# Optimization experiments

Measured on AMD Instinct MI355X. Metric: run time of the kernel, lower is better.

## Reference

```python
import jax, jax.numpy as jnp
import numpy as np

N_NODES = 89250
N_EDGES = 899756
IN_F = 500
HID = 256
N_CLS = 7


def setup_inputs() -> dict:
    key = jax.random.key(0)
    ks = jax.random.split(key, 12)
    x = jax.random.normal(ks[0], (N_NODES, IN_F), dtype=jnp.float32)
    edge_index = jax.random.randint(ks[1], (2, N_EDGES), 0, N_NODES, dtype=jnp.int32)
    edge_weight = jax.random.uniform(ks[2], (N_EDGES,), dtype=jnp.float32)
    def glorot(k, shape):
        fan_in, fan_out = shape
        s = (6.0 / (fan_in + fan_out)) ** 0.5
        return jax.random.uniform(k, shape, jnp.float32, -s, s)
    W1 = glorot(ks[3], (2 * IN_F, HID))
    b1 = jnp.zeros((HID,), jnp.float32)
    W2 = glorot(ks[4], (2 * HID, HID))
    b2 = jnp.zeros((HID,), jnp.float32)
    W3 = glorot(ks[5], (2 * HID, HID))
    b3 = jnp.zeros((HID,), jnp.float32)
    Wl = glorot(ks[6], (3 * HID, N_CLS))
    bl = jnp.zeros((N_CLS,), jnp.float32)
    return {"x": x, "edge_index": edge_index, "edge_weight": edge_weight,
            "W1": W1, "b1": b1, "W2": W2, "b2": b2, "W3": W3, "b3": b3,
            "Wl": Wl, "bl": bl}


def _sage_conv(x, src, dst, edge_weight, W, b, num_nodes):
    # legacy PyG SAGEConv(concat=True): mean-aggregate weighted neighbor msgs,
    # concat with root features, then single linear (2*in -> out). No self-loops.
    msg = x[src] * edge_weight[:, None]                                  # [E, F]
    agg = jax.ops.segment_sum(msg, dst, num_segments=num_nodes)          # [N, F]
    cnt = jax.ops.segment_sum(jnp.ones_like(edge_weight), dst, num_segments=num_nodes)
    agg = agg / jnp.maximum(cnt, 1.0)[:, None]                           # scatter_mean
    h = jnp.concatenate([x, agg], axis=-1)                               # [N, 2F]
    return h @ W + b


def reference(x, edge_index, edge_weight, W1, b1, W2, b2, W3, b3, Wl, bl):
    n = x.shape[0]
    src, dst = edge_index[0], edge_index[1]  # message flows source -> target
    x1 = jax.nn.relu(_sage_conv(x, src, dst, edge_weight, W1, b1, n))
    x2 = jax.nn.relu(_sage_conv(x1, src, dst, edge_weight, W2, b2, n))
    x3 = jax.nn.relu(_sage_conv(x2, src, dst, edge_weight, W3, b3, n))
    h = jnp.concatenate([x1, x2, x3], axis=-1)                            # [N, 3H]
    logits = h @ Wl + bl                                                  # [N, C]
    return jax.nn.log_softmax(logits, axis=-1)
```

## Files before the change

### kernel.cpp

```cpp
#include <hip/hip_runtime.h>
#include <hip/hip_bf16.h>

#define NN 89250
#define NE 899756
#define INF_ 500
#define HID 256
#define NCLS 7

typedef __attribute__((ext_vector_type(8))) short bf16x8;
typedef __attribute__((ext_vector_type(4))) float f32x4;

#define GL2LDS16(gp, lp)                                                        \
    __builtin_amdgcn_global_load_lds(                                           \
        (const __attribute__((address_space(1))) void*)(gp),                    \
        (__attribute__((address_space(3))) void*)(lp), 16, 0, 0)

static __device__ __forceinline__ float b2f(short s) {
    union { unsigned int u; float f; } v;
    v.u = ((unsigned int)(unsigned short)s) << 16;
    return v.f;
}

__global__ void hist_kernel(const int* __restrict__ dst, int* __restrict__ cnt, int E) {
    int e = blockIdx.x * 256 + threadIdx.x;
    if (e < E) atomicAdd(&cnt[dst[e]], 1);
}

__global__ __launch_bounds__(256) void scan1_kernel(const int* __restrict__ cnt,
                                                    int* __restrict__ loc,
                                                    int* __restrict__ bsum, int N) {
    __shared__ int sd[256];
    int b = blockIdx.x, tid = threadIdx.x;
    int base = b * 1024 + tid * 4;
    int v[4];
    int sum = 0;
#pragma unroll
    for (int k = 0; k < 4; k++) {
        int i = base + k;
        v[k] = (i < N) ? cnt[i] : 0;
        sum += v[k];
    }
    sd[tid] = sum;
    __syncthreads();
    for (int off = 1; off < 256; off <<= 1) {
        int add = (tid >= off) ? sd[tid - off] : 0;
        __syncthreads();
        sd[tid] += add;
        __syncthreads();
    }
    int run = sd[tid] - sum;
    if (tid == 255) bsum[b] = sd[255];
#pragma unroll
    for (int k = 0; k < 4; k++) {
        int i = base + k;
        if (i < N) loc[i] = run;
        run += v[k];
    }
}

__global__ __launch_bounds__(256) void scan2_kernel(int* __restrict__ bsum,
                                                    int* __restrict__ total, int nb) {
    __shared__ int sd[256];
    int tid = threadIdx.x;
    int v = (tid < nb) ? bsum[tid] : 0;
    sd[tid] = v;
    __syncthreads();
    for (int off = 1; off < 256; off <<= 1) {
        int add = (tid >= off) ? sd[tid - off] : 0;
        __syncthreads();
        sd[tid] += add;
        __syncthreads();
    }
    if (tid < nb) bsum[tid] = sd[tid] - v;
    if (tid == 255) *total = sd[255];
}

__global__ void scan3_kernel(const int* __restrict__ cnt, const int* __restrict__ loc,
                             const int* __restrict__ bsum, const int* __restrict__ total,
                             int* __restrict__ offs, int* __restrict__ cursor,
                             float* __restrict__ invc, int N) {
    int i = blockIdx.x * 256 + threadIdx.x;
    if (i < N) {
        int o = loc[i] + bsum[i >> 10];
        offs[i] = o;
        cursor[i] = o;
        invc[i] = 1.0f / fmaxf((float)cnt[i], 1.0f);
    }
    if (i == 0) offs[N] = *total;
}

__global__ void scatter_kernel(const int* __restrict__ src, const int* __restrict__ dst,
                               const float* __restrict__ w, int* __restrict__ cursor,
                               int* __restrict__ csr_src, float* __restrict__ csr_w, int E) {
    int e = blockIdx.x * 256 + threadIdx.x;
    if (e < E) {
        int d = dst[e];
        int pos = atomicAdd(&cursor[d], 1);
        csr_src[pos] = src[e];
        csr_w[pos] = w[e];
    }
}

__global__ void conv_x_kernel(const float* __restrict__ x, __hip_bfloat16* __restrict__ xb) {
    long long idx = (long long)blockIdx.x * 256 + threadIdx.x;
    if (idx >= (long long)NN * 128) return;
    int row = (int)(idx >> 7), slot = (int)(idx & 127);
    float4 v = make_float4(0.f, 0.f, 0.f, 0.f);
    if (slot < 125) v = *(const float4*)&x[(size_t)row * 500 + slot * 4];
    __hip_bfloat16* o = xb + (size_t)row * 512 + slot * 4;
    o[0] = __float2bfloat16(v.x);
    o[1] = __float2bfloat16(v.y);
    o[2] = __float2bfloat16(v.z);
    o[3] = __float2bfloat16(v.w);
}

__global__ void conv_w_kernel(const float* __restrict__ W, __hip_bfloat16* __restrict__ BT,
                              int K, int Kp) {
    int idx = blockIdx.x * 256 + threadIdx.x;
    if (idx >= 512 * Kp) return;
    int j = idx / Kp, k = idx - j * Kp;
    float v = (k < K) ? W[(size_t)(k + ((j >= 256) ? K : 0)) * 256 + (j & 255)] : 0.f;
    BT[idx] = __float2bfloat16(v);
}

__global__ __launch_bounds__(256, 2) void gemm_mfma(
    const __hip_bfloat16* __restrict__ A, const __hip_bfloat16* __restrict__ BT,
    const float* __restrict__ bias, float* __restrict__ S,
    __hip_bfloat16* __restrict__ T, int N, int K) {
    __shared__ short lA[128 * 64];
    __shared__ short lB[128 * 64];
    int tid = threadIdx.x;
    int row0 = blockIdx.x * 128;
    int col0 = blockIdx.y * 128;
    int w = tid >> 6, l = tid & 63;
    int wm = (w >> 1) * 64, wn = (w & 1) * 64;
    int lr = l & 15, lk = (l >> 4) * 8;

    const char* gA[4];
    const char* gB[4];
    int ls[4];
#pragma unroll
    for (int p = 0; p < 4; p++) {
        int s = tid + p * 256;
        int r = s >> 3, c = s & 7;
        int ga_row = row0 + r;
        if (ga_row > N - 1) ga_row = N - 1;
        gA[p] = (const char*)A + (size_t)ga_row * K * 2 + c * 16;
        gB[p] = (const char*)BT + (size_t)(col0 + r) * K * 2 + c * 16;
        ls[p] = s * 16;
    }

    f32x4 acc[4][4];
#pragma unroll
    for (int m = 0; m < 4; m++)
#pragma unroll
        for (int n = 0; n < 4; n++) acc[m][n] = (f32x4){0.f, 0.f, 0.f, 0.f};

    int KT = K >> 6;
    for (int kt = 0; kt < KT; kt++) {
        size_t koff = (size_t)kt * 128;
#pragma unroll
        for (int p = 0; p < 4; p++) GL2LDS16(gA[p] + koff, (char*)lA + ls[p]);
#pragma unroll
        for (int p = 0; p < 4; p++) GL2LDS16(gB[p] + koff, (char*)lB + ls[p]);
        __syncthreads();
#pragma unroll
        for (int kk = 0; kk < 64; kk += 32) {
            bf16x8 af[4], bfr[4];
#pragma unroll
            for (int m = 0; m < 4; m++)
                af[m] = *(const bf16x8*)&lA[(wm + m * 16 + lr) * 64 + kk + lk];
#pragma unroll
            for (int n = 0; n < 4; n++)
                bfr[n] = *(const bf16x8*)&lB[(wn + n * 16 + lr) * 64 + kk + lk];
#pragma unroll
            for (int m = 0; m < 4; m++)
#pragma unroll
                for (int n = 0; n < 4; n++)
                    acc[m][n] = __builtin_amdgcn_mfma_f32_16x16x32_bf16(af[m], bfr[n],
                                                                        acc[m][n], 0, 0, 0);
        }
        __syncthreads();
    }

    int crow_base = row0 + wm + (l >> 4) * 4;
    bool isT = (col0 >= 256);
#pragma unroll
    for (int n = 0; n < 4; n++) {
        int col = col0 + wn + n * 16 + lr;
        float bv = isT ? 0.f : bias[col];
#pragma unroll
        for (int m = 0; m < 4; m++) {
#pragma unroll
            for (int r = 0; r < 4; r++) {
                int row = crow_base + m * 16 + r;
                if (row < N) {
                    float v = acc[m][n][r] + bv;
                    if (isT)
                        T[(size_t)row * 256 + (col - 256)] = __float2bfloat16(v);
                    else
                        S[(size_t)row * 256 + col] = v;
                }
            }
        }
    }
}

__global__ __launch_bounds__(256) void agg_fused_kernel(
    const float* __restrict__ S, const __hip_bfloat16* __restrict__ T,
    const int* __restrict__ offs, const int* __restrict__ csr_src,
    const float* __restrict__ csr_w, const float* __restrict__ invc,
    const float* __restrict__ Wlc, __hip_bfloat16* __restrict__ act,
    float* __restrict__ logits, int N) {
    __shared__ float sW[HID * NCLS];
    for (int i = threadIdx.x; i < HID * NCLS; i += 256) sW[i] = Wlc[i];
    __syncthreads();

    int g = threadIdx.x >> 5, t = threadIdx.x & 31;
    int n = blockIdx.x * 8 + g;
    if (n >= N) return;
    int beg = offs[n], end = offs[n + 1];

    float acc[8] = {};
    int j = beg;
    for (; j + 4 <= end; j += 4) {
        int s0 = csr_src[j], s1 = csr_src[j + 1], s2 = csr_src[j + 2], s3 = csr_src[j + 3];
        float w0 = csr_w[j], w1 = csr_w[j + 1], w2 = csr_w[j + 2], w3 = csr_w[j + 3];
        bf16x8 r0 = *(const bf16x8*)&T[(size_t)s0 * 256 + t * 8];
        bf16x8 r1 = *(const bf16x8*)&T[(size_t)s1 * 256 + t * 8];
        bf16x8 r2 = *(const bf16x8*)&T[(size_t)s2 * 256 + t * 8];
        bf16x8 r3 = *(const bf16x8*)&T[(size_t)s3 * 256 + t * 8];
#pragma unroll
        for (int k = 0; k < 8; k++) {
            acc[k] += b2f(r0[k]) * w0;
            acc[k] += b2f(r1[k]) * w1;
            acc[k] += b2f(r2[k]) * w2;
            acc[k] += b2f(r3[k]) * w3;
        }
    }
    for (; j < end; j++) {
        int s0 = csr_src[j];
        float w0 = csr_w[j];
        bf16x8 r0 = *(const bf16x8*)&T[(size_t)s0 * 256 + t * 8];
#pragma unroll
        for (int k = 0; k < 8; k++) acc[k] += b2f(r0[k]) * w0;
    }

    float ic = invc[n];
    const float* Srow = S + (size_t)n * 256 + t * 8;
    float4 sv0 = *(const float4*)&Srow[0];
    float4 sv1 = *(const float4*)&Srow[4];
    float a[8];
    a[0] = fmaxf(sv0.x + acc[0] * ic, 0.f);
    a[1] = fmaxf(sv0.y + acc[1] * ic, 0.f);
    a[2] = fmaxf(sv0.z + acc[2] * ic, 0.f);
    a[3] = fmaxf(sv0.w + acc[3] * ic, 0.f);
    a[4] = fmaxf(sv1.x + acc[4] * ic, 0.f);
    a[5] = fmaxf(sv1.y + acc[5] * ic, 0.f);
    a[6] = fmaxf(sv1.z + acc[6] * ic, 0.f);
    a[7] = fmaxf(sv1.w + acc[7] * ic, 0.f);

    bf16x8 ov;
#pragma unroll
    for (int k = 0; k < 8; k++) {
        __hip_bfloat16 h = __float2bfloat16(a[k]);
        ov[k] = *reinterpret_cast<short*>(&h);
    }
    *(bf16x8*)&act[(size_t)n * 256 + t * 8] = ov;

    float pl[NCLS] = {};
#pragma unroll
    for (int k = 0; k < 8; k++) {
        int f = t * 8 + k;
        float av = a[k];
#pragma unroll
        for (int c = 0; c < NCLS; c++) pl[c] += av * sW[f * NCLS + c];
    }
#pragma unroll
    for (int c = 0; c < NCLS; c++) {
#pragma unroll
        for (int off = 16; off >= 1; off >>= 1) pl[c] += __shfl_xor(pl[c], off, 32);
    }
    if (t == 0) {
        float* lp = logits + (size_t)n * NCLS;
#pragma unroll
        for (int c = 0; c < NCLS; c++) lp[c] += pl[c];
    }
}

__global__ void logsoftmax_kernel(const float* __restrict__ logits, const float* __restrict__ bl,
                                  float* __restrict__ out, int N) {
    int n = blockIdx.x * 256 + threadIdx.x;
    if (n >= N) return;
    float l[NCLS];
    float m = -1e30f;
#pragma unroll
    for (int c = 0; c < NCLS; c++) {
        l[c] = logits[(size_t)n * NCLS + c] + bl[c];
        m = fmaxf(m, l[c]);
    }
    float s = 0.f;
#pragma unroll
    for (int c = 0; c < NCLS; c++) s += expf(l[c] - m);
    float lse = m + logf(s);
#pragma unroll
    for (int c = 0; c < NCLS; c++) out[(size_t)n * NCLS + c] = l[c] - lse;
}

extern "C" void kernel_launch(void* const* d_in, const int* in_sizes, int n_in,
                              void* d_out, int out_size, void* d_ws, size_t ws_size,
                              hipStream_t stream) {
    const float* x  = (const float*)d_in[0];
    const int*   ei = (const int*)d_in[1];
    const float* ew = (const float*)d_in[2];
    const float* W1 = (const float*)d_in[3];
    const float* b1 = (const float*)d_in[4];
    const float* W2 = (const float*)d_in[5];
    const float* b2 = (const float*)d_in[6];
    const float* W3 = (const float*)d_in[7];
    const float* b3 = (const float*)d_in[8];
    const float* Wl = (const float*)d_in[9];
    const float* bl = (const float*)d_in[10];
    float* out = (float*)d_out;

    const int N = NN, E = NE;
    const int* src = ei;
    const int* dst = ei + E;

    char* p = (char*)d_ws;
    auto alloc = [&](size_t bytes) {
        void* r = (void*)p;
        p += (bytes + 255) & ~(size_t)255;
        return r;
    };
    float*          S      = (float*)alloc((size_t)N * 256 * 4);
    __hip_bfloat16* T      = (__hip_bfloat16*)alloc((size_t)N * 256 * 2);
    __hip_bfloat16* act    = (__hip_bfloat16*)alloc((size_t)N * 256 * 2);
    __hip_bfloat16* xbf    = (__hip_bfloat16*)alloc((size_t)N * 512 * 2);
    __hip_bfloat16* B1T    = (__hip_bfloat16*)alloc((size_t)512 * 512 * 2);
    __hip_bfloat16* B2T    = (__hip_bfloat16*)alloc((size_t)512 * 256 * 2);
    __hip_bfloat16* B3T    = (__hip_bfloat16*)alloc((size_t)512 * 256 * 2);
    float*          logits = (float*)alloc((size_t)N * NCLS * 4);
    int*            cnt    = (int*)alloc((size_t)N * 4);
    int*            offs   = (int*)alloc((size_t)(N + 1) * 4);
    int*            cursor = (int*)alloc((size_t)N * 4);
    float*          invc   = (float*)alloc((size_t)N * 4);
    int*            loc    = (int*)alloc((size_t)N * 4);
    int*            bsum   = (int*)alloc(256 * 4);
    int*            total  = (int*)alloc(4);
    int*            csr_src = (int*)alloc((size_t)E * 4);
    float*          csr_w   = (float*)alloc((size_t)E * 4);

    hipMemsetAsync(cnt, 0, (size_t)N * 4, stream);
    hipMemsetAsync(logits, 0, (size_t)N * NCLS * 4, stream);

    int nb = (N + 1023) / 1024;
    hist_kernel<<<(E + 255) / 256, 256, 0, stream>>>(dst, cnt, E);
    scan1_kernel<<<nb, 256, 0, stream>>>(cnt, loc, bsum, N);
    scan2_kernel<<<1, 256, 0, stream>>>(bsum, total, nb);
    scan3_kernel<<<(N + 255) / 256, 256, 0, stream>>>(cnt, loc, bsum, total, offs, cursor, invc, N);
    scatter_kernel<<<(E + 255) / 256, 256, 0, stream>>>(src, dst, ew, cursor, csr_src, csr_w, E);

    conv_x_kernel<<<(int)(((long long)N * 128 + 255) / 256), 256, 0, stream>>>(x, xbf);
    conv_w_kernel<<<(512 * 512 + 255) / 256, 256, 0, stream>>>(W1, B1T, INF_, 512);
    conv_w_kernel<<<(512 * 256 + 255) / 256, 256, 0, stream>>>(W2, B2T, HID, 256);
    conv_w_kernel<<<(512 * 256 + 255) / 256, 256, 0, stream>>>(W3, B3T, HID, 256);

    dim3 ggrid((N + 127) / 128, 4);
    int agrid = (N + 7) / 8;

    gemm_mfma<<<ggrid, 256, 0, stream>>>(xbf, B1T, b1, S, T, N, 512);
    agg_fused_kernel<<<agrid, 256, 0, stream>>>(S, T, offs, csr_src, csr_w, invc,
                                                Wl, act, logits, N);
    gemm_mfma<<<ggrid, 256, 0, stream>>>(act, B2T, b2, S, T, N, 256);
    agg_fused_kernel<<<agrid, 256, 0, stream>>>(S, T, offs, csr_src, csr_w, invc,
                                                Wl + (size_t)HID * NCLS, act, logits, N);
    gemm_mfma<<<ggrid, 256, 0, stream>>>(act, B3T, b3, S, T, N, 256);
    agg_fused_kernel<<<agrid, 256, 0, stream>>>(S, T, offs, csr_src, csr_w, invc,
                                                Wl + (size_t)2 * HID * NCLS, act, logits, N);

    logsoftmax_kernel<<<(N + 255) / 256, 256, 0, stream>>>(logits, bl, out, N);
}
```

Baseline: 975.9 us.

## Store self-term in bf16, remap GEMM blocks per XCD, unroll gather by 8

The self-projection buffer S becomes bf16 instead of fp32, which halves its write and read traffic between the GEMM and the aggregation kernel. The GEMM switches to a 1D grid with an XCD-aware block remap, so the four column tiles of a row panel run on the same die and share the A rows in L2. The neighbour-gather loop is unrolled from 4 to 8 edges to keep more loads in flight. The bf16 rounding of S adds some numeric error, and the remap assumes the grid size divides by 8.

```diff
diff --git a/kernel.cpp b/kernel.cpp
--- a/kernel.cpp
+++ b/kernel.cpp
@@ -125,13 +125,16 @@
 
 __global__ __launch_bounds__(256, 2) void gemm_mfma(
     const __hip_bfloat16* __restrict__ A, const __hip_bfloat16* __restrict__ BT,
-    const float* __restrict__ bias, float* __restrict__ S,
+    const float* __restrict__ bias, __hip_bfloat16* __restrict__ S,
     __hip_bfloat16* __restrict__ T, int N, int K) {
     __shared__ short lA[128 * 64];
     __shared__ short lB[128 * 64];
     int tid = threadIdx.x;
-    int row0 = blockIdx.x * 128;
-    int col0 = blockIdx.y * 128;
+    int chunk = gridDim.x >> 3;
+    int bid = blockIdx.x;
+    int logical = (bid & 7) * chunk + (bid >> 3);
+    int row0 = (logical >> 2) * 128;
+    int col0 = (logical & 3) * 128;
     int w = tid >> 6, l = tid & 63;
     int wm = (w >> 1) * 64, wn = (w & 1) * 64;
     int lr = l & 15, lk = (l >> 4) * 8;
@@ -189,6 +192,7 @@
     for (int n = 0; n < 4; n++) {
         int col = col0 + wn + n * 16 + lr;
         float bv = isT ? 0.f : bias[col];
+        int ocol = col & 255;
 #pragma unroll
         for (int m = 0; m < 4; m++) {
 #pragma unroll
@@ -197,9 +201,9 @@
                 if (row < N) {
                     float v = acc[m][n][r] + bv;
                     if (isT)
-                        T[(size_t)row * 256 + (col - 256)] = __float2bfloat16(v);
+                        T[(size_t)row * 256 + ocol] = __float2bfloat16(v);
                     else
-                        S[(size_t)row * 256 + col] = v;
+                        S[(size_t)row * 256 + ocol] = __float2bfloat16(v);
                 }
             }
         }
@@ -207,7 +211,7 @@
 }
 
 __global__ __launch_bounds__(256) void agg_fused_kernel(
-    const float* __restrict__ S, const __hip_bfloat16* __restrict__ T,
+    const __hip_bfloat16* __restrict__ S, const __hip_bfloat16* __restrict__ T,
     const int* __restrict__ offs, const int* __restrict__ csr_src,
     const float* __restrict__ csr_w, const float* __restrict__ invc,
     const float* __restrict__ Wlc, __hip_bfloat16* __restrict__ act,
@@ -223,20 +227,21 @@
 
     float acc[8] = {};
     int j = beg;
-    for (; j + 4 <= end; j += 4) {
-        int s0 = csr_src[j], s1 = csr_src[j + 1], s2 = csr_src[j + 2], s3 = csr_src[j + 3];
-        float w0 = csr_w[j], w1 = csr_w[j + 1], w2 = csr_w[j + 2], w3 = csr_w[j + 3];
-        bf16x8 r0 = *(const bf16x8*)&T[(size_t)s0 * 256 + t * 8];
-        bf16x8 r1 = *(const bf16x8*)&T[(size_t)s1 * 256 + t * 8];
-        bf16x8 r2 = *(const bf16x8*)&T[(size_t)s2 * 256 + t * 8];
-        bf16x8 r3 = *(const bf16x8*)&T[(size_t)s3 * 256 + t * 8];
-#pragma unroll
-        for (int k = 0; k < 8; k++) {
-            acc[k] += b2f(r0[k]) * w0;
-            acc[k] += b2f(r1[k]) * w1;
-            acc[k] += b2f(r2[k]) * w2;
-            acc[k] += b2f(r3[k]) * w3;
+    for (; j + 8 <= end; j += 8) {
+        int ss[8];
+        float ww[8];
+#pragma unroll
+        for (int u = 0; u < 8; u++) {
+            ss[u] = csr_src[j + u];
+            ww[u] = csr_w[j + u];
         }
+        bf16x8 rr[8];
+#pragma unroll
+        for (int u = 0; u < 8; u++) rr[u] = *(const bf16x8*)&T[(size_t)ss[u] * 256 + t * 8];
+#pragma unroll
+        for (int u = 0; u < 8; u++)
+#pragma unroll
+            for (int k = 0; k < 8; k++) acc[k] += b2f(rr[u][k]) * ww[u];
     }
     for (; j < end; j++) {
         int s0 = csr_src[j];
@@ -247,18 +252,10 @@
     }
 
     float ic = invc[n];
-    const float* Srow = S + (size_t)n * 256 + t * 8;
-    float4 sv0 = *(const float4*)&Srow[0];
-    float4 sv1 = *(const float4*)&Srow[4];
+    bf16x8 sv = *(const bf16x8*)&S[(size_t)n * 256 + t * 8];
     float a[8];
-    a[0] = fmaxf(sv0.x + acc[0] * ic, 0.f);
-    a[1] = fmaxf(sv0.y + acc[1] * ic, 0.f);
-    a[2] = fmaxf(sv0.z + acc[2] * ic, 0.f);
-    a[3] = fmaxf(sv0.w + acc[3] * ic, 0.f);
-    a[4] = fmaxf(sv1.x + acc[4] * ic, 0.f);
-    a[5] = fmaxf(sv1.y + acc[5] * ic, 0.f);
-    a[6] = fmaxf(sv1.z + acc[6] * ic, 0.f);
-    a[7] = fmaxf(sv1.w + acc[7] * ic, 0.f);
+#pragma unroll
+    for (int k = 0; k < 8; k++) a[k] = fmaxf(b2f(sv[k]) + acc[k] * ic, 0.f);
 
     bf16x8 ov;
 #pragma unroll
@@ -333,7 +330,7 @@
         p += (bytes + 255) & ~(size_t)255;
         return r;
     };
-    float*          S      = (float*)alloc((size_t)N * 256 * 4);
+    __hip_bfloat16* S      = (__hip_bfloat16*)alloc((size_t)N * 256 * 2);
     __hip_bfloat16* T      = (__hip_bfloat16*)alloc((size_t)N * 256 * 2);
     __hip_bfloat16* act    = (__hip_bfloat16*)alloc((size_t)N * 256 * 2);
     __hip_bfloat16* xbf    = (__hip_bfloat16*)alloc((size_t)N * 512 * 2);
@@ -366,16 +363,16 @@
     conv_w_kernel<<<(512 * 256 + 255) / 256, 256, 0, stream>>>(W2, B2T, HID, 256);
     conv_w_kernel<<<(512 * 256 + 255) / 256, 256, 0, stream>>>(W3, B3T, HID, 256);
 
-    dim3 ggrid((N + 127) / 128, 4);
+    int nwg = ((N + 127) / 128) * 4;
     int agrid = (N + 7) / 8;
 
-    gemm_mfma<<<ggrid, 256, 0, stream>>>(xbf, B1T, b1, S, T, N, 512);
+    gemm_mfma<<<nwg, 256, 0, stream>>>(xbf, B1T, b1, S, T, N, 512);
     agg_fused_kernel<<<agrid, 256, 0, stream>>>(S, T, offs, csr_src, csr_w, invc,
                                                 Wl, act, logits, N);
-    gemm_mfma<<<ggrid, 256, 0, stream>>>(act, B2T, b2, S, T, N, 256);
+    gemm_mfma<<<nwg, 256, 0, stream>>>(act, B2T, b2, S, T, N, 256);
     agg_fused_kernel<<<agrid, 256, 0, stream>>>(S, T, offs, csr_src, csr_w, invc,
                                                 Wl + (size_t)HID * NCLS, act, logits, N);
-    gemm_mfma<<<ggrid, 256, 0, stream>>>(act, B3T, b3, S, T, N, 256);
+    gemm_mfma<<<nwg, 256, 0, stream>>>(act, B3T, b3, S, T, N, 256);
     agg_fused_kernel<<<agrid, 256, 0, stream>>>(S, T, offs, csr_src, csr_w, invc,
                                                 Wl + (size_t)2 * HID * NCLS, act, logits, N);
 
```

Result: no change. 992.9 us (+1.7%).
